# Kernel optimization log

Measured on AMD Instinct MI355X. Metric: run time of the kernel, lower is better.

The kernel has to match this reference:

```python
import jax, jax.numpy as jnp
import numpy as np

C = 10  # cluster gap window; repo-level global constant in the original code


def _per_neuron(v, label):
    """Faithful vectorized translation of the per-(batch,neuron) Python loops.

    v:     [T] membrane potential trace
    label: scalar int target cluster count
    Returns (loss_contribution, num_cluster).
    """
    T = v.shape[0]
    t = jnp.arange(T, dtype=jnp.int32)
    spk = v >= 0.0                                   # spike positions (v >= 0)
    # exclusive prefix counts of spikes: csp[i] = #spikes in v[:i]
    csp = jnp.concatenate([jnp.zeros(1, jnp.int32), jnp.cumsum(spk.astype(jnp.int32))])
    lo = jnp.clip(t - C, 0, T)
    # a spike starts a new cluster iff no spike in the preceding C steps
    cnt_prev = csp[t] - csp[lo]
    is_start = spk & (cnt_prev == 0)
    num_cluster = jnp.sum(is_start.astype(jnp.int32))
    vmax = jnp.max(v)

    # ---- excess branch (label > num_cluster) ----
    # mask[t] = 1 iff some spike lies in [t-C, t+C]  (union of [first-C, last+C] per cluster)
    hi = jnp.clip(t + C + 1, 0, T)
    mask = (csp[hi] - csp[lo]) > 0
    full0 = jnp.all(mask)
    NEG = jnp.asarray(-1e30, v.dtype)
    m0 = jnp.max(jnp.where(mask, NEG, v))            # max over unmasked times (iter 0)
    tm = jnp.argmax(v)                               # original uses global argmax of v
    win = (t >= tm - C // 2) & (t <= tm + C // 2)
    mask2 = mask | win                               # mask after first loop iteration (fixed thereafter)
    full2 = jnp.all(mask2)
    # if mask2 full, remaining iterations pick a spike value (random in original; spikes have v>=0,
    # we use the deterministic surrogate vmax which is always a spike value when spikes exist)
    m_rest = jnp.where(full2, vmax, jnp.max(jnp.where(mask2, NEG, v)))
    label_f = label.astype(v.dtype)
    ncf = num_cluster.astype(v.dtype)
    dE = jnp.maximum(label_f - ncf, 1.0)             # safe denominator (branch-gated below)
    mean_excess = (m0 + (dE - 1.0) * m_rest) / dE
    excess_loss = jnp.where(full0, vmax, -mean_excess)

    # ---- deficit branch (label < num_cluster) ----
    BIG = T + 2 * C + 2
    lt = jax.lax.cummax(jnp.where(spk, t, -BIG))                 # nearest spike <= t
    rt = jax.lax.cummin(jnp.where(spk, t, BIG)[::-1])[::-1]      # nearest spike >= t
    in_span = (rt - lt) <= C                                     # t inside [first,last] of a cluster
    cid = jnp.cumsum(is_start.astype(jnp.int32)) - 1             # cluster id at time t
    K = T // (C + 1) + 1                                         # max possible clusters
    seg = jnp.where(in_span, cid, K)
    rec = jax.ops.segment_max(v, seg, num_segments=K + 1)[:K]    # per-cluster span max
    POS = jnp.asarray(1e30, v.dtype)
    rec = jnp.where(jnp.arange(K) < num_cluster, rec, POS)
    rec = jnp.sort(rec)                                          # ascending, real clusters first
    dD = jnp.maximum(ncf - label_f, 1.0)
    deficit_loss = jnp.sum(jnp.where(jnp.arange(K) < (num_cluster - label), rec, 0.0)) / dD

    contrib = jnp.where(label > num_cluster, excess_loss,
                        jnp.where(label < num_cluster, deficit_loss, 0.0))
    return contrib, num_cluster


def setup_inputs() -> dict:
    key = jax.random.key(0)
    k1, k2, k3 = jax.random.split(key, 3)
    B, T, N = 256, 500, 128
    vmem = jax.random.normal(k1, (B, T, N), dtype=jnp.float32)
    vlastmem = jax.random.normal(k2, (B, T, N), dtype=jnp.float32)
    labels_t = jax.random.randint(k3, (B, N), 0, 5, dtype=jnp.int32)
    return {"vmem": vmem, "vlastmem": vlastmem, "labels_t": labels_t, "ratio": 1}


def reference(vmem, vlastmem, labels_t, ratio):
    # vlastmem and ratio are unused in the original forward; kept for signature fidelity.
    vv = jnp.transpose(vmem, (0, 2, 1))  # [B, N, T]
    contrib, nclus = jax.vmap(jax.vmap(_per_neuron))(vv, labels_t)
    loss = jnp.sum(contrib)
    spike_output = nclus.astype(jnp.float32)  # [B, N] cluster counts
    return loss, spike_output
```

## Files before the change

### kernel.cpp

```cpp
#include <hip/hip_runtime.h>

namespace {
constexpr int CC    = 10;
constexpr int TT    = 500;
constexpr int NN    = 128;
constexpr int G     = 10;
constexpr int LSEG  = TT / G;
constexpr int HALO  = CC;
constexpr int NSLOT = 10;
constexpr int MAXG  = TT / (CC + 1) + 1;
}

__global__ __launch_bounds__(128, 5)
void seg_scan_kernel(const float* __restrict__ vmem, float* __restrict__ ws) {
    const int s   = blockIdx.x;
    const int b   = blockIdx.y;
    const int tid = threadIdx.x;
    const int a   = s * LSEG;
    const float* __restrict__ col = vmem + (size_t)b * TT * NN + tid;

    __shared__ float stg[5 * NN];

    float b0[10], b1[10], b2[10], b3[10] = {};
    auto load = [&](float (&d)[10], int c) {
        #pragma unroll
        for (int j = 0; j < 10; ++j) {
            int t = a + (-HALO + 10 * c + j);
            t = t < 0 ? 0 : (t > TT - 1 ? TT - 1 : t);
            d[j] = col[(size_t)t * NN];
        }
    };

    int   ls = -(1 << 20), lcount = 0, hdne = 0, tmn = 0, hasu = 0;
    float ccm = -1e30f, rmax = -1e30f, hdm = -1e30f, vmx = -1e30f, m0 = -1e30f;
    const bool firstSeg = (s == 0), lastSeg = (s == G - 1);
    #pragma unroll
    for (int i = 0; i < 5; ++i) stg[i * NN + tid] = 0.0f;

    auto scan = [&](const float (&cur)[10], const float (&prev)[10], int c) {
        #pragma unroll
        for (int j = 0; j < 10; ++j) {
            const int ofs = -HALO + 10 * c + j;
            const int t   = a + ofs;
            float v = cur[j];
            if ((ofs < 0 && firstSeg) || (ofs >= LSEG && lastSeg)) v = -1.0f;
            const bool spike = v >= 0.0f;
            if (ofs >= 0 && ofs < LSEG) {
                const float rm2 = fmaxf(rmax, v);
                if (spike) {
                    if (t - ls > CC) {
                        if (lcount > 0) stg[(lcount - 1) * NN + tid] = ccm;
                        ccm = v; ++lcount;
                    } else if (lcount == 0) { hdne = 1; hdm = fmaxf(hdm, rm2); }
                    else ccm = fmaxf(ccm, rm2);
                    rmax = -1e30f;
                } else rmax = rm2;
                if (v > vmx) { vmx = v; tmn = t; }
            }
            if (spike) ls = t;
            if (ofs >= HALO) {
                const float vu = prev[j];
                if (ls < t - 2 * CC) { hasu = 1; if (vu > m0) m0 = vu; }
            }
        }
    };

    load(b0, 0); load(b1, 1);
    load(b2, 2); scan(b0, b3, 0);
    load(b3, 3); scan(b1, b0, 1);
    load(b0, 4); scan(b2, b1, 2);
    load(b1, 5); scan(b3, b2, 3);
    load(b2, 6); scan(b0, b3, 4);
    scan(b1, b0, 5);
    scan(b2, b1, 6);

    if (lcount > 0) stg[(lcount - 1) * NN + tid] = ccm;

    float* __restrict__ wsl = ws + (size_t)(b * G + s) * NSLOT * NN + tid;
    #pragma unroll
    for (int i = 0; i < 5; ++i) wsl[i * NN] = stg[i * NN + tid];
    const int packed = lcount | (hdne << 3) | (hasu << 4) | (tmn << 5);
    wsl[5 * NN] = __int_as_float(packed);
    wsl[6 * NN] = hdm;
    wsl[7 * NN] = rmax;
    wsl[8 * NN] = vmx;
    wsl[9 * NN] = m0;
}

__global__ __launch_bounds__(64)
void merge_kernel(const float* __restrict__ vmem, const float* __restrict__ ws,
                  const int* __restrict__ labels, float* __restrict__ out) {
    const int bb = blockIdx.x, lane = threadIdx.x;
    const int b = bb >> 1, n = ((bb & 1) << 6) | lane;
    __shared__ float gl[MAXG * 64];
    __shared__ float wb[512];

    const float* __restrict__ wsb = ws + (size_t)b * G * NSLOT * NN + n;
    float f[2][10];
    auto loadSeg = [&](int slot, int s2) {
        const float* p = wsb + (size_t)s2 * NSLOT * NN;
        #pragma unroll
        for (int i = 0; i < 10; ++i) f[slot][i] = p[i * NN];
    };
    loadSeg(0, 0);

    int g = 0, g_nc = 0, g_hasu = 0, g_tm = 0;
    bool open = false; float cur = -1e30f, ptg = -1e30f;
    float g_vmax = -1e30f, g_m0 = -1e30f;
    #pragma unroll
    for (int s2 = 0; s2 < G; ++s2) {
        if (s2 + 1 < G) loadSeg((s2 + 1) & 1, s2 + 1);
        const float (&d)[10] = f[s2 & 1];
        const int pk = __float_as_int(d[5]);
        const int k = pk & 7, hne = (pk >> 3) & 1;
        g_nc += k; g_hasu |= (pk >> 4) & 1;
        if (d[8] > g_vmax) { g_vmax = d[8]; g_tm = pk >> 5; }
        if (d[9] > g_m0) g_m0 = d[9];
        if (open) {
            if (hne) { cur = fmaxf(cur, fmaxf(ptg, d[6])); ptg = d[7]; }
            if (k > 0 || !hne) { gl[g * 64 + lane] = cur; ++g; open = false; }
        }
        if (k > 0) {
            #pragma unroll
            for (int i = 0; i < 4; ++i)
                if (i < k - 1) { gl[g * 64 + lane] = d[i]; ++g; }
            float last = d[4];
            if (k == 1) last = d[0];
            else if (k == 2) last = d[1];
            else if (k == 3) last = d[2];
            else if (k == 4) last = d[3];
            cur = last; open = true; ptg = d[7];
        }
    }
    if (open) { gl[g * 64 + lane] = cur; ++g; }

    const int label = labels[b * NN + n];

    const bool need2 = (label > g_nc) && g_hasu && (label - g_nc >= 2);
    float mrest = g_vmax;
    unsigned long long bal = __ballot(need2);
    const float* colbase = vmem + (size_t)b * TT * NN;
    while (bal) {
        const int fl = __ffsll((unsigned long long)bal) - 1;
        bal &= bal - 1;
        const int   nf    = ((bb & 1) << 6) | fl;
        const int   tmf   = __shfl(g_tm, fl);
        const float vmaxf = __shfl(g_vmax, fl);
        #pragma unroll
        for (int j = 0; j < 8; ++j) {
            const int t = lane * 8 + j;
            wb[t] = (t < TT) ? colbase[(size_t)t * NN + nf] : -1.0f;
        }
        __syncthreads();
        int ls2 = -1000, lh = 0; float lm = -1e30f;
        const int u0 = lane * 8;
        for (int t2 = u0 - 10; t2 < u0 + 18; ++t2) {
            const float v = (t2 >= 0 && t2 < 512) ? wb[t2] : -1.0f;
            if (v >= 0.0f) ls2 = t2;
            const int u = t2 - 10;
            if (u >= u0 && u < u0 + 8 && u < TT) {
                if (ls2 < u - 10 && (u < tmf - CC / 2 || u > tmf + CC / 2)) {
                    lh = 1; const float vu = wb[u]; if (vu > lm) lm = vu;
                }
            }
        }
        #pragma unroll
        for (int off = 32; off > 0; off >>= 1) {
            lm = fmaxf(lm, __shfl_down(lm, off));
            lh |= __shfl_down(lh, off);
        }
        const float res = __shfl(lh ? lm : vmaxf, 0);
        if (lane == fl) mrest = res;
        __syncthreads();
    }

    float contrib = 0.0f;
    if (label > g_nc) {
        if (!g_hasu) contrib = g_vmax;
        else {
            const float dE = (float)(label - g_nc);
            contrib = -((g_m0 + (dE - 1.0f) * mrest) / dE);
        }
    } else if (label < g_nc) {
        const int kk = g_nc - label;
        float ssum = 0.0f;
        for (int i = 0; i < kk; ++i) {
            float mn = 1e30f; int mj = 0;
            for (int jj = 0; jj < g_nc; ++jj) {
                const float x = gl[jj * 64 + lane];
                if (x < mn) { mn = x; mj = jj; }
            }
            ssum += mn; gl[mj * 64 + lane] = 1e30f;
        }
        contrib = ssum / (float)kk;
    }

    out[1 + b * NN + n] = (float)g_nc;

    float w = contrib;
    #pragma unroll
    for (int off = 32; off > 0; off >>= 1) w += __shfl_down(w, off);
    if (lane == 0) atomicAdd(out, w);
}

extern "C" void kernel_launch(void* const* d_in, const int* in_sizes, int n_in,
                              void* d_out, int out_size, void* d_ws, size_t ws_size,
                              hipStream_t stream) {
    const float* vmem   = (const float*)d_in[0];
    const int*   labels = (const int*)d_in[2];
    float*       out    = (float*)d_out;
    float*       ws     = (float*)d_ws;

    const int B = in_sizes[2] / NN;

    hipMemsetAsync(out, 0, sizeof(float), stream);
    hipLaunchKernelGGL(seg_scan_kernel, dim3(G, B), dim3(NN), 0, stream, vmem, ws);
    hipLaunchKernelGGL(merge_kernel, dim3(2 * B), dim3(64), 0, stream, vmem, ws, labels, out);
}
```

Measured before the change: 163.6 us.

## Preload full segment into registers, widen merge blocks, drop memset launch

The segment scan now issues all 70 column loads up front into one register array behind a scheduling barrier, replacing the rotating four-buffer software pipeline, and lowers the occupancy hint. The merge kernel moves from 64-thread to 256-thread blocks, each covering two batches. It preloads all 100 workspace values per thread, swaps block syncs for wave barriers, and reduces to one atomic per block. The output zeroing moves into the first kernel, removing the memset launch. Together these aim to raise memory-level parallelism and cut launch and atomic overhead, at the cost of higher register pressure and possible spills.

```diff
diff --git a/kernel.cpp b/kernel.cpp
--- a/kernel.cpp
+++ b/kernel.cpp
@@ -9,27 +9,30 @@
 constexpr int HALO  = CC;
 constexpr int NSLOT = 10;
 constexpr int MAXG  = TT / (CC + 1) + 1;
-}
-
-__global__ __launch_bounds__(128, 5)
-void seg_scan_kernel(const float* __restrict__ vmem, float* __restrict__ ws) {
+constexpr int NELEM = LSEG + 2 * HALO;
+}
+
+__global__ __launch_bounds__(128, 4)
+void seg_scan_kernel(const float* __restrict__ vmem, float* __restrict__ ws,
+                     float* __restrict__ out) {
     const int s   = blockIdx.x;
     const int b   = blockIdx.y;
     const int tid = threadIdx.x;
     const int a   = s * LSEG;
-    const float* __restrict__ col = vmem + (size_t)b * TT * NN + tid;
+    const float* __restrict__ col = vmem + b * TT * NN + tid;
+
+    if (s == 0 && b == 0 && tid == 0) out[0] = 0.0f;
 
     __shared__ float stg[5 * NN];
 
-    float b0[10], b1[10], b2[10], b3[10] = {};
-    auto load = [&](float (&d)[10], int c) {
-        #pragma unroll
-        for (int j = 0; j < 10; ++j) {
-            int t = a + (-HALO + 10 * c + j);
-            t = t < 0 ? 0 : (t > TT - 1 ? TT - 1 : t);
-            d[j] = col[(size_t)t * NN];
-        }
-    };
+    float r[NELEM];
+    #pragma unroll
+    for (int i = 0; i < NELEM; ++i) {
+        int t = a + i - HALO;
+        t = t < 0 ? 0 : (t > TT - 1 ? TT - 1 : t);
+        r[i] = col[t * NN];
+    }
+    __builtin_amdgcn_sched_barrier(0);
 
     int   ls = -(1 << 20), lcount = 0, hdne = 0, tmn = 0, hasu = 0;
     float ccm = -1e30f, rmax = -1e30f, hdm = -1e30f, vmx = -1e30f, m0 = -1e30f;
@@ -37,43 +40,31 @@
     #pragma unroll
     for (int i = 0; i < 5; ++i) stg[i * NN + tid] = 0.0f;
 
-    auto scan = [&](const float (&cur)[10], const float (&prev)[10], int c) {
-        #pragma unroll
-        for (int j = 0; j < 10; ++j) {
-            const int ofs = -HALO + 10 * c + j;
-            const int t   = a + ofs;
-            float v = cur[j];
-            if ((ofs < 0 && firstSeg) || (ofs >= LSEG && lastSeg)) v = -1.0f;
-            const bool spike = v >= 0.0f;
-            if (ofs >= 0 && ofs < LSEG) {
-                const float rm2 = fmaxf(rmax, v);
-                if (spike) {
-                    if (t - ls > CC) {
-                        if (lcount > 0) stg[(lcount - 1) * NN + tid] = ccm;
-                        ccm = v; ++lcount;
-                    } else if (lcount == 0) { hdne = 1; hdm = fmaxf(hdm, rm2); }
-                    else ccm = fmaxf(ccm, rm2);
-                    rmax = -1e30f;
-                } else rmax = rm2;
-                if (v > vmx) { vmx = v; tmn = t; }
-            }
-            if (spike) ls = t;
-            if (ofs >= HALO) {
-                const float vu = prev[j];
-                if (ls < t - 2 * CC) { hasu = 1; if (vu > m0) m0 = vu; }
-            }
-        }
-    };
-
-    load(b0, 0); load(b1, 1);
-    load(b2, 2); scan(b0, b3, 0);
-    load(b3, 3); scan(b1, b0, 1);
-    load(b0, 4); scan(b2, b1, 2);
-    load(b1, 5); scan(b3, b2, 3);
-    load(b2, 6); scan(b0, b3, 4);
-    scan(b1, b0, 5);
-    scan(b2, b1, 6);
-
+    #pragma unroll
+    for (int i = 0; i < NELEM; ++i) {
+        const int ofs = i - HALO;
+        const int t   = a + ofs;
+        float v = r[i];
+        if ((ofs < 0 && firstSeg) || (ofs >= LSEG && lastSeg)) v = -1.0f;
+        const bool spike = v >= 0.0f;
+        if (ofs >= 0 && ofs < LSEG) {
+            const float rm2 = fmaxf(rmax, v);
+            if (spike) {
+                if (t - ls > CC) {
+                    if (lcount > 0) stg[(lcount - 1) * NN + tid] = ccm;
+                    ccm = v; ++lcount;
+                } else if (lcount == 0) { hdne = 1; hdm = fmaxf(hdm, rm2); }
+                else ccm = fmaxf(ccm, rm2);
+                rmax = -1e30f;
+            } else rmax = rm2;
+            if (v > vmx) { vmx = v; tmn = t; }
+        }
+        if (spike) ls = t;
+        if (ofs >= HALO) {
+            const float vu = r[i - 10];
+            if (ls < t - 2 * CC) { hasu = 1; if (vu > m0) m0 = vu; }
+        }
+    }
     if (lcount > 0) stg[(lcount - 1) * NN + tid] = ccm;
 
     float* __restrict__ wsl = ws + (size_t)(b * G + s) * NSLOT * NN + tid;
@@ -87,30 +78,33 @@
     wsl[9 * NN] = m0;
 }
 
-__global__ __launch_bounds__(64)
+__global__ __launch_bounds__(256, 1)
 void merge_kernel(const float* __restrict__ vmem, const float* __restrict__ ws,
                   const int* __restrict__ labels, float* __restrict__ out) {
-    const int bb = blockIdx.x, lane = threadIdx.x;
-    const int b = bb >> 1, n = ((bb & 1) << 6) | lane;
-    __shared__ float gl[MAXG * 64];
-    __shared__ float wb[512];
+    const int tid  = threadIdx.x;
+    const int lane = tid & 63;
+    const int wv   = tid >> 6;
+    const int b    = blockIdx.x * 2 + (tid >> 7);
+    const int n    = tid & 127;
+
+    __shared__ float gl[MAXG * 256];
+    __shared__ float wb[4][512];
+    __shared__ float red[4];
 
     const float* __restrict__ wsb = ws + (size_t)b * G * NSLOT * NN + n;
-    float f[2][10];
-    auto loadSeg = [&](int slot, int s2) {
-        const float* p = wsb + (size_t)s2 * NSLOT * NN;
-        #pragma unroll
-        for (int i = 0; i < 10; ++i) f[slot][i] = p[i * NN];
-    };
-    loadSeg(0, 0);
+    float f[G * NSLOT];
+    #pragma unroll
+    for (int k = 0; k < G * NSLOT; ++k) f[k] = wsb[(size_t)k * NN];
+    __builtin_amdgcn_sched_barrier(0);
+
+    const int label = labels[b * NN + n];
 
     int g = 0, g_nc = 0, g_hasu = 0, g_tm = 0;
     bool open = false; float cur = -1e30f, ptg = -1e30f;
     float g_vmax = -1e30f, g_m0 = -1e30f;
     #pragma unroll
     for (int s2 = 0; s2 < G; ++s2) {
-        if (s2 + 1 < G) loadSeg((s2 + 1) & 1, s2 + 1);
-        const float (&d)[10] = f[s2 & 1];
+        const float* d = &f[s2 * NSLOT];
         const int pk = __float_as_int(d[5]);
         const int k = pk & 7, hne = (pk >> 3) & 1;
         g_nc += k; g_hasu |= (pk >> 4) & 1;
@@ -118,12 +112,12 @@
         if (d[9] > g_m0) g_m0 = d[9];
         if (open) {
             if (hne) { cur = fmaxf(cur, fmaxf(ptg, d[6])); ptg = d[7]; }
-            if (k > 0 || !hne) { gl[g * 64 + lane] = cur; ++g; open = false; }
+            if (k > 0 || !hne) { gl[g * 256 + tid] = cur; ++g; open = false; }
         }
         if (k > 0) {
             #pragma unroll
             for (int i = 0; i < 4; ++i)
-                if (i < k - 1) { gl[g * 64 + lane] = d[i]; ++g; }
+                if (i < k - 1) { gl[g * 256 + tid] = d[i]; ++g; }
             float last = d[4];
             if (k == 1) last = d[0];
             else if (k == 2) last = d[1];
@@ -132,35 +126,35 @@
             cur = last; open = true; ptg = d[7];
         }
     }
-    if (open) { gl[g * 64 + lane] = cur; ++g; }
-
-    const int label = labels[b * NN + n];
+    if (open) { gl[g * 256 + tid] = cur; ++g; }
 
     const bool need2 = (label > g_nc) && g_hasu && (label - g_nc >= 2);
     float mrest = g_vmax;
     unsigned long long bal = __ballot(need2);
     const float* colbase = vmem + (size_t)b * TT * NN;
+    float* __restrict__ wbp = wb[wv];
     while (bal) {
         const int fl = __ffsll((unsigned long long)bal) - 1;
         bal &= bal - 1;
-        const int   nf    = ((bb & 1) << 6) | fl;
+        const int   nf    = ((wv & 1) << 6) | fl;
         const int   tmf   = __shfl(g_tm, fl);
         const float vmaxf = __shfl(g_vmax, fl);
         #pragma unroll
         for (int j = 0; j < 8; ++j) {
             const int t = lane * 8 + j;
-            wb[t] = (t < TT) ? colbase[(size_t)t * NN + nf] : -1.0f;
-        }
-        __syncthreads();
+            wbp[t] = (t < TT) ? colbase[(size_t)t * NN + nf] : -1.0f;
+        }
+        asm volatile("s_waitcnt lgkmcnt(0)" ::: "memory");
+        __builtin_amdgcn_wave_barrier();
         int ls2 = -1000, lh = 0; float lm = -1e30f;
         const int u0 = lane * 8;
         for (int t2 = u0 - 10; t2 < u0 + 18; ++t2) {
-            const float v = (t2 >= 0 && t2 < 512) ? wb[t2] : -1.0f;
+            const float v = (t2 >= 0 && t2 < 512) ? wbp[t2] : -1.0f;
             if (v >= 0.0f) ls2 = t2;
             const int u = t2 - 10;
             if (u >= u0 && u < u0 + 8 && u < TT) {
                 if (ls2 < u - 10 && (u < tmf - CC / 2 || u > tmf + CC / 2)) {
-                    lh = 1; const float vu = wb[u]; if (vu > lm) lm = vu;
+                    lh = 1; const float vu = wbp[u]; if (vu > lm) lm = vu;
                 }
             }
         }
@@ -171,7 +165,7 @@
         }
         const float res = __shfl(lh ? lm : vmaxf, 0);
         if (lane == fl) mrest = res;
-        __syncthreads();
+        __builtin_amdgcn_wave_barrier();
     }
 
     float contrib = 0.0f;
@@ -187,10 +181,10 @@
         for (int i = 0; i < kk; ++i) {
             float mn = 1e30f; int mj = 0;
             for (int jj = 0; jj < g_nc; ++jj) {
-                const float x = gl[jj * 64 + lane];
+                const float x = gl[jj * 256 + tid];
                 if (x < mn) { mn = x; mj = jj; }
             }
-            ssum += mn; gl[mj * 64 + lane] = 1e30f;
+            ssum += mn; gl[mj * 256 + tid] = 1e30f;
         }
         contrib = ssum / (float)kk;
     }
@@ -200,7 +194,9 @@
     float w = contrib;
     #pragma unroll
     for (int off = 32; off > 0; off >>= 1) w += __shfl_down(w, off);
-    if (lane == 0) atomicAdd(out, w);
+    if (lane == 0) red[wv] = w;
+    __syncthreads();
+    if (tid == 0) atomicAdd(out, red[0] + red[1] + red[2] + red[3]);
 }
 
 extern "C" void kernel_launch(void* const* d_in, const int* in_sizes, int n_in,
@@ -213,7 +209,6 @@
 
     const int B = in_sizes[2] / NN;
 
-    hipMemsetAsync(out, 0, sizeof(float), stream);
-    hipLaunchKernelGGL(seg_scan_kernel, dim3(G, B), dim3(NN), 0, stream, vmem, ws);
-    hipLaunchKernelGGL(merge_kernel, dim3(2 * B), dim3(64), 0, stream, vmem, ws, labels, out);
-}
+    hipLaunchKernelGGL(seg_scan_kernel, dim3(G, B), dim3(NN), 0, stream, vmem, ws, out);
+    hipLaunchKernelGGL(merge_kernel, dim3(B / 2), dim3(256), 0, stream, vmem, ws, labels, out);
+}
```

Result: no change. 161.9 us (-1.0%).
